# Kernel optimization log

Hardware: AMD Instinct MI355X
Metric: run time of the kernel (lower is better)

The kernel has to match this reference:

```python
import jax, jax.numpy as jnp
import numpy as np

GAMMA = 0.1
C = 0.0
B, L = 16, 2048


def setup_inputs() -> dict:
    key = jax.random.key(0)
    k1, k2, k3 = jax.random.split(key, 3)
    inputs = jax.random.normal(k1, (B, L), dtype=jnp.float32)
    target = jax.random.randint(k2, (B, L), 0, 2, dtype=jnp.int32)
    # label frequencies (positive counts)
    freq = jax.random.uniform(k3, (L,), dtype=jnp.float32) * 999.0 + 1.0
    return {"input": inputs, "target": target, "freq": freq}


def reference(input, target, freq):
    # Masked, fully-vectorized equivalent of the per-sample masked_select +
    # roll pairwise loss. For each sample, the rolls enumerate all ordered
    # (pos_a, pos_b) pairs, so:
    #   loss1 = sum_{a,b pos} relu( (f_a - f_b)/(f_a + f_b) * (x_a - x_b) )
    #   loss2 = gamma * sum_{a pos, j neg} relu( x_j - x_a + c )
    x = jax.nn.sigmoid(input)                      # [B, L]
    pos = target.astype(x.dtype)                    # [B, L]
    neg = 1.0 - pos

    # batch-independent pairwise frequency factor  [L, L]
    n = (freq[:, None] - freq[None, :]) / (freq[:, None] + freq[None, :])

    diff = x[:, :, None] - x[:, None, :]            # [B, L, L]: x_a - x_j
    pp = pos[:, :, None] * pos[:, None, :]          # pos-pos pair mask
    pn = pos[:, :, None] * neg[:, None, :]          # pos-neg pair mask

    term = jax.nn.relu(n[None] * diff) * pp + GAMMA * jax.nn.relu(C - diff) * pn
    return jnp.sum(term) / x.shape[0]
```

## Files before the change

kernel.cpp:

```cpp
#include <hip/hip_runtime.h>

#define L 2048
#define B 16
#define TPB 256
#define BPR 64
#define A_PER_BLOCK (L / BPR)
#define J_ITERS (L / TPB)
#define GAMMA 0.1f

__global__ __launch_bounds__(TPB) void pair_loss_kernel(
    const float* __restrict__ input, const int* __restrict__ target,
    const float* __restrict__ freq, float* __restrict__ partial) {
  __shared__ float2 xf[L];
  __shared__ float red[TPB / 64];

  const int b = blockIdx.x / BPR;
  const int chunk = blockIdx.x % BPR;
  const float* row = input + b * L;
  const int* trow = target + b * L;

  for (int j = threadIdx.x; j < L; j += TPB) {
    float v = row[j];
    float x = 1.0f / (1.0f + __expf(-v));
    float f = freq[j];
    xf[j] = make_float2(x, trow[j] ? f : -f);
  }
  __syncthreads();

  float acc = 0.0f;
  const int a0 = chunk * A_PER_BLOCK;
  for (int ai = 0; ai < A_PER_BLOCK; ++ai) {
    float2 af = xf[a0 + ai];
    if (af.y < 0.0f) continue;
    const float xa = af.x, fa = af.y;
#pragma unroll
    for (int jj = 0; jj < J_ITERS; ++jj) {
      float2 v = xf[jj * TPB + threadIdx.x];
      float fj = fabsf(v.y);
      float d  = xa - v.x;
      float p  = (fa - fj) * d;
      float t1 = fmaxf(p, 0.0f) * __builtin_amdgcn_rcpf(fa + fj);
      float t2 = GAMMA * fmaxf(-d, 0.0f);
      acc += (v.y > 0.0f) ? t1 : t2;
    }
  }

#pragma unroll
  for (int off = 32; off; off >>= 1) acc += __shfl_down(acc, off, 64);
  if ((threadIdx.x & 63) == 0) red[threadIdx.x >> 6] = acc;
  __syncthreads();
  if (threadIdx.x == 0) {
    float s = 0.0f;
#pragma unroll
    for (int w = 0; w < TPB / 64; ++w) s += red[w];
    partial[blockIdx.x] = s;
  }
}

__global__ __launch_bounds__(TPB) void reduce_kernel(
    const float* __restrict__ partial, float* __restrict__ out, int n) {
  float acc = 0.0f;
  for (int i = threadIdx.x; i < n; i += TPB) acc += partial[i];
#pragma unroll
  for (int off = 32; off; off >>= 1) acc += __shfl_down(acc, off, 64);
  __shared__ float red[TPB / 64];
  if ((threadIdx.x & 63) == 0) red[threadIdx.x >> 6] = acc;
  __syncthreads();
  if (threadIdx.x == 0) {
    float s = 0.0f;
#pragma unroll
    for (int w = 0; w < TPB / 64; ++w) s += red[w];
    out[0] = s * (1.0f / (float)B);
  }
}

extern "C" void kernel_launch(void* const* d_in, const int* in_sizes, int n_in,
                              void* d_out, int out_size, void* d_ws, size_t ws_size,
                              hipStream_t stream) {
  const float* input  = (const float*)d_in[0];
  const int*   target = (const int*)d_in[1];
  const float* freq   = (const float*)d_in[2];
  float* out = (float*)d_out;
  float* partial = (float*)d_ws;

  const int nblocks = B * BPR;
  pair_loss_kernel<<<nblocks, TPB, 0, stream>>>(input, target, freq, partial);
  reduce_kernel<<<1, TPB, 0, stream>>>(partial, out, nblocks);
}
```

Before: 77.54 us.

## Compact positive and negative elements in shared memory to balance pair work

The staging loop now uses wave ballots and shared atomics to split each row into a packed positive array (x, freq) and a packed negative array (x). Each block then takes an even share of the positive anchors and loops only over the compacted positives and negatives. This removes the per-element select and sign check, drops the wasted rcp and mul work on pairs that are discarded, and balances anchors across blocks. The cost is an atomic-based compaction step and inner loops whose trip counts are no longer known at compile time. Summation order also becomes nondeterministic because the compaction order depends on the atomics.

Measured after the change: 72.90 us. 6.0% less time.

```diff
diff --git a/kernel.cpp b/kernel.cpp
--- a/kernel.cpp
+++ b/kernel.cpp
@@ -4,52 +4,71 @@
 #define B 16
 #define TPB 256
 #define BPR 64
-#define A_PER_BLOCK (L / BPR)
-#define J_ITERS (L / TPB)
 #define GAMMA 0.1f
 
 __global__ __launch_bounds__(TPB) void pair_loss_kernel(
     const float* __restrict__ input, const int* __restrict__ target,
     const float* __restrict__ freq, float* __restrict__ partial) {
-  __shared__ float2 xf[L];
+  __shared__ float2 pf[L];
+  __shared__ float nx[L];
+  __shared__ int cnt[2];
   __shared__ float red[TPB / 64];
 
   const int b = blockIdx.x / BPR;
   const int chunk = blockIdx.x % BPR;
+  const int tid = threadIdx.x;
+  const int lane = tid & 63;
+
+  if (tid < 2) cnt[tid] = 0;
+  __syncthreads();
+
   const float* row = input + b * L;
   const int* trow = target + b * L;
 
-  for (int j = threadIdx.x; j < L; j += TPB) {
+  for (int j = tid; j < L; j += TPB) {
     float v = row[j];
     float x = 1.0f / (1.0f + __expf(-v));
     float f = freq[j];
-    xf[j] = make_float2(x, trow[j] ? f : -f);
+    bool pos = trow[j] != 0;
+    unsigned long long mp = __ballot(pos);
+    unsigned long long lowmask = (1ull << lane) - 1ull;
+    int pcnt = __popcll(mp);
+    int pbase, nbase;
+    if (lane == 0) {
+      pbase = atomicAdd(&cnt[0], pcnt);
+      nbase = atomicAdd(&cnt[1], 64 - pcnt);
+    }
+    pbase = __shfl(pbase, 0, 64);
+    nbase = __shfl(nbase, 0, 64);
+    if (pos) pf[pbase + __popcll(mp & lowmask)] = make_float2(x, f);
+    else     nx[nbase + __popcll(~mp & lowmask)] = x;
   }
   __syncthreads();
 
-  float acc = 0.0f;
-  const int a0 = chunk * A_PER_BLOCK;
-  for (int ai = 0; ai < A_PER_BLOCK; ++ai) {
-    float2 af = xf[a0 + ai];
-    if (af.y < 0.0f) continue;
+  const int np = cnt[0], nn = cnt[1];
+  const int a0 = (chunk * np) / BPR;
+  const int a1 = ((chunk + 1) * np) / BPR;
+
+  float accp = 0.0f, accn = 0.0f;
+  for (int a = a0; a < a1; ++a) {
+    float2 af = pf[a];
     const float xa = af.x, fa = af.y;
-#pragma unroll
-    for (int jj = 0; jj < J_ITERS; ++jj) {
-      float2 v = xf[jj * TPB + threadIdx.x];
-      float fj = fabsf(v.y);
-      float d  = xa - v.x;
-      float p  = (fa - fj) * d;
-      float t1 = fmaxf(p, 0.0f) * __builtin_amdgcn_rcpf(fa + fj);
-      float t2 = GAMMA * fmaxf(-d, 0.0f);
-      acc += (v.y > 0.0f) ? t1 : t2;
+    for (int j = tid; j < np; j += TPB) {
+      float2 v = pf[j];
+      float t = fmaxf((fa - v.y) * (xa - v.x), 0.0f);
+      accp += t * __builtin_amdgcn_rcpf(fa + v.y);
+    }
+    for (int j = tid; j < nn; j += TPB) {
+      accn += fmaxf(nx[j] - xa, 0.0f);
     }
   }
+  float acc = accp + GAMMA * accn;
 
 #pragma unroll
   for (int off = 32; off; off >>= 1) acc += __shfl_down(acc, off, 64);
-  if ((threadIdx.x & 63) == 0) red[threadIdx.x >> 6] = acc;
+  if (lane == 0) red[tid >> 6] = acc;
   __syncthreads();
-  if (threadIdx.x == 0) {
+  if (tid == 0) {
     float s = 0.0f;
 #pragma unroll
     for (int w = 0; w < TPB / 64; ++w) s += red[w];
```
